# Kernel optimization log

Measured on AMD Instinct MI355X. Metric: run time of the kernel, lower is better.

Reference implementation:

```python
import jax, jax.numpy as jnp
import numpy as np

N = 100000      # nodes
E = 1600000     # edges
F = 64          # num_features
C = 10          # num_classes
L = 4           # num_layers
B = 128         # graphs in batch


def setup_inputs() -> dict:
    key = jax.random.key(0)
    ks = jax.random.split(key, 8)
    x = jax.random.normal(ks[0], (N, F), dtype=jnp.float32)
    edge_index = jax.random.randint(ks[1], (2, E), 0, N, dtype=jnp.int64)
    batch = jnp.sort(jax.random.randint(ks[2], (N,), 0, B, dtype=jnp.int64))
    scale = 1.0 / jnp.sqrt(jnp.float32(F))
    W1s = jax.random.normal(ks[3], (L, F, F), dtype=jnp.float32) * scale
    W2s = jax.random.normal(ks[4], (L, F, F), dtype=jnp.float32) * scale
    fc_w = jax.random.normal(ks[5], (C, F), dtype=jnp.float32) * scale
    fc_b = jax.random.normal(ks[6], (C,), dtype=jnp.float32) * 0.01
    return {"x": x, "edge_index": edge_index, "batch": batch,
            "W1s": W1s, "W2s": W2s, "fc_w": fc_w, "fc_b": fc_b}


def reference(x, edge_index, batch, W1s, W2s, fc_w, fc_b):
    src, dst = edge_index[0], edge_index[1]
    h = x
    for l in range(L):  # small fixed layer count
        # GINConv, eps=0: (1+eps)*x + sum of neighbor features (gather + scatter-add)
        agg = jax.ops.segment_sum(h[src], dst, num_segments=N)
        h = agg + h
        # MLP([F,F,F], bias=False, plain_last=False, act=sigmoid): two linears, each followed by sigmoid
        h = jax.nn.sigmoid(h @ W1s[l])
        h = jax.nn.sigmoid(h @ W2s[l])
    # global_add_pool over graphs in the batch
    xr = jax.ops.segment_sum(h, batch, num_segments=B)  # [B, F]
    logits = xr @ fc_w.T + fc_b                          # [B, C]
    return jax.nn.log_softmax(logits, axis=1), xr
```

## Files before the change

### kernel.cpp

```cpp
#include <hip/hip_runtime.h>
#include <hip/hip_bf16.h>

#define NN 100000
#define NE 1600000
#define FF 64
#define NC 10
#define NL 4
#define NB 128
#define LDST 72
#define CAP 48
#define NW 196
#define WCAPE 8704
#define PB_BIN 196
#define PB_XF 782
#define PB_W 32
#define PB_TOTAL (PB_BIN + PB_XF + PB_W + 1)
#define LAYER_BLOCKS ((NN + 15) / 16)

typedef __attribute__((ext_vector_type(8))) short short8;
typedef __attribute__((ext_vector_type(8))) unsigned short ushort8;
typedef __attribute__((ext_vector_type(4))) float f32x4;
typedef __attribute__((ext_vector_type(2))) float f32x2;
typedef __attribute__((ext_vector_type(4))) int int4v;

static __device__ __forceinline__ unsigned short f2bf(float x) {
  unsigned int u = __float_as_uint(x);
  unsigned int r = (u + 0x7fffu + ((u >> 16) & 1u)) >> 16;
  return (unsigned short)r;
}
static __device__ __forceinline__ float bf2f(unsigned short u) {
  return __uint_as_float(((unsigned int)u) << 16);
}
static __device__ __forceinline__ uint2 pack_f8(const float* a) {
  int w0 = __builtin_amdgcn_cvt_pk_fp8_f32(a[0], a[1], 0, false);
  w0 = __builtin_amdgcn_cvt_pk_fp8_f32(a[2], a[3], w0, true);
  int w1 = __builtin_amdgcn_cvt_pk_fp8_f32(a[4], a[5], 0, false);
  w1 = __builtin_amdgcn_cvt_pk_fp8_f32(a[6], a[7], w1, true);
  return make_uint2((unsigned)w0, (unsigned)w1);
}
static __device__ __forceinline__ void acc8w(f32x2* a, unsigned int x,
                                             unsigned int y) {
#if __has_builtin(__builtin_amdgcn_cvt_pk_f32_fp8)
  a[0] += __builtin_amdgcn_cvt_pk_f32_fp8((int)x, false);
  a[1] += __builtin_amdgcn_cvt_pk_f32_fp8((int)x, true);
  a[2] += __builtin_amdgcn_cvt_pk_f32_fp8((int)y, false);
  a[3] += __builtin_amdgcn_cvt_pk_f32_fp8((int)y, true);
#else
  a[0][0] += __builtin_amdgcn_cvt_f32_fp8((int)x, 0);
  a[0][1] += __builtin_amdgcn_cvt_f32_fp8((int)x, 1);
  a[1][0] += __builtin_amdgcn_cvt_f32_fp8((int)x, 2);
  a[1][1] += __builtin_amdgcn_cvt_f32_fp8((int)x, 3);
  a[2][0] += __builtin_amdgcn_cvt_f32_fp8((int)y, 0);
  a[2][1] += __builtin_amdgcn_cvt_f32_fp8((int)y, 1);
  a[3][0] += __builtin_amdgcn_cvt_f32_fp8((int)y, 2);
  a[3][1] += __builtin_amdgcn_cvt_f32_fp8((int)y, 3);
#endif
}
static __device__ __forceinline__ void acc16(f32x2* a, uint4 v) {
  acc8w(a, v.x, v.y);
  acc8w(a + 4, v.z, v.w);
}
static __device__ __forceinline__ void nacc(unsigned& pe0, unsigned& po0,
                                            unsigned& pe1, unsigned& po1,
                                            uint2 r) {
  pe0 += r.x & 0x0F0F0F0Fu; po0 += (r.x >> 4) & 0x0F0F0F0Fu;
  pe1 += r.y & 0x0F0F0F0Fu; po1 += (r.y >> 4) & 0x0F0F0F0Fu;
}

__global__ __launch_bounds__(1024) void prepbin_kernel(
    const float* __restrict__ x, const int* __restrict__ src,
    const int* __restrict__ dst, const float* __restrict__ W1s,
    const float* __restrict__ W2s, uint2* __restrict__ xf8,
    unsigned short* __restrict__ Wt, int* __restrict__ wcnt,
    unsigned int* __restrict__ ebuf, unsigned char* __restrict__ hq0,
    unsigned char* __restrict__ hq1) {
  __shared__ int lcnt[NW];
  __shared__ int lbase[NW];
  int b = blockIdx.x;
  int t = threadIdx.x;
  if (b < PB_BIN) {
    int base = b * 8192 + t * 8;
    int d[8], s[8], wj[8], p8[8];
    bool v[8];
    if (base + 8 <= NE) {
      *(int4*)(&d[0]) = *(const int4*)(dst + base);
      *(int4*)(&d[4]) = *(const int4*)(dst + base + 4);
      *(int4*)(&s[0]) = *(const int4*)(src + base);
      *(int4*)(&s[4]) = *(const int4*)(src + base + 4);
      #pragma unroll
      for (int j = 0; j < 8; ++j) v[j] = true;
    } else {
      #pragma unroll
      for (int j = 0; j < 8; ++j) {
        int e = base + j;
        v[j] = (e < NE);
        d[j] = v[j] ? dst[e] : 0;
        s[j] = v[j] ? src[e] : 0;
      }
    }
    #pragma unroll
    for (int j = 0; j < 8; ++j) wj[j] = d[j] >> 9;
    if (t < NW) lcnt[t] = 0;
    __syncthreads();
    #pragma unroll
    for (int j = 0; j < 8; ++j)
      if (v[j]) p8[j] = atomicAdd(&lcnt[wj[j]], 1);
    __syncthreads();
    if (t < NW) lbase[t] = atomicAdd(&wcnt[t], lcnt[t]);
    __syncthreads();
    #pragma unroll
    for (int j = 0; j < 8; ++j) {
      if (v[j]) {
        int pos = lbase[wj[j]] + p8[j];
        if (pos < WCAPE)
          ebuf[(size_t)wj[j] * WCAPE + pos] =
              ((unsigned)(d[j] & 511) << 17) | (unsigned)s[j];
      }
    }
  } else if (b < PB_BIN + PB_XF) {
    int g = (b - PB_BIN) * 1024 + t;
    if (g < NN * FF / 8) {
      size_t base = (size_t)g * 8;
      float4 a = *(const float4*)(x + base);
      float4 c = *(const float4*)(x + base + 4);
      float f[8] = {a.x, a.y, a.z, a.w, c.x, c.y, c.z, c.w};
      xf8[g] = pack_f8(f);
    }
  } else if (b < PB_BIN + PB_XF + PB_W) {
    int g = (b - PB_BIN - PB_XF) * 1024 + t;
    int mat = g >> 12, idx = g & 4095;
    int k = idx >> 6, n = idx & 63;
    int l = mat >> 1;
    const float* W = (mat & 1) ? (W2s + (size_t)l * FF * FF) : (W1s + (size_t)l * FF * FF);
    Wt[(size_t)mat * FF * FF + n * FF + k] = f2bf(W[k * FF + n]);
  } else {
    if (t < 8) {
      xf8[(size_t)NN * 8 + t] = make_uint2(0, 0);
    } else if (t < 12) {
      ((uint2*)hq0)[(size_t)NN * 4 + (t - 8)] = make_uint2(0, 0);
    } else if (t < 16) {
      ((uint2*)hq1)[(size_t)NN * 4 + (t - 12)] = make_uint2(0, 0);
    }
  }
}

__global__ __launch_bounds__(1024) void fillC_kernel(const unsigned int* __restrict__ ebuf,
                                                     const int* __restrict__ wcnt,
                                                     int* __restrict__ csr,
                                                     int* __restrict__ deg) {
  __shared__ int cur[512];
  int b = blockIdx.x;
  int t = threadIdx.x;
  int n0 = b << 9;
  if (t < 512) cur[t] = 0;
  __syncthreads();
  int cnt = min(wcnt[b], WCAPE);
  const unsigned int* ep = ebuf + (size_t)b * WCAPE;
  for (int i = t; i < cnt; i += 1024) {
    unsigned int e = ep[i];
    int dl = e >> 17;
    int s = (int)(e & 0x1ffffu);
    int slot = atomicAdd(&cur[dl], 1);
    if (slot < CAP) csr[(n0 + dl) * CAP + slot] = s;
  }
  __syncthreads();
  if (t < 512) {
    int node = n0 + t;
    if (node < NN) {
      int c = min(cur[t], CAP);
      deg[node] = c;
      int end = (c + 3) & ~3;
      for (; c < end; ++c) csr[node * CAP + c] = NN;
    }
  }
}

template <int IN4>
__global__ __launch_bounds__(64) void layer_kernel(
    const void* __restrict__ hin, const int* __restrict__ csr,
    const int* __restrict__ deg, const unsigned short* __restrict__ Wt,
    unsigned char* __restrict__ hout4, const int* __restrict__ batch,
    float* __restrict__ xr, int last) {
  __shared__ __align__(16) unsigned short uL[16 * LDST];
  __shared__ __align__(16) unsigned char fb[16 * 64];
  int lane = threadIdx.x;
  int row0 = blockIdx.x * 16;
  int j2 = lane & 3;
  int gnode = lane >> 2;

  {
    int r = gnode;
    int node = row0 + r;
    ushort8 u0, u1;
    if (IN4) {
      float af[16];
      #pragma unroll
      for (int k = 0; k < 16; ++k) af[k] = 0.f;
      if (node < NN) {
        const uint2* hb = (const uint2*)hin;
        uint2 sv = hb[(size_t)node * 4 + j2];
        unsigned se0 = sv.x & 0x0F0F0F0Fu, so0 = (sv.x >> 4) & 0x0F0F0F0Fu;
        unsigned se1 = sv.y & 0x0F0F0F0Fu, so1 = (sv.y >> 4) & 0x0F0F0F0Fu;
        #pragma unroll
        for (int k = 0; k < 4; ++k) {
          af[2 * k]         = (float)((se0 >> (8 * k)) & 0xFFu);
          af[2 * k + 1]     = (float)((so0 >> (8 * k)) & 0xFFu);
          af[8 + 2 * k]     = (float)((se1 >> (8 * k)) & 0xFFu);
          af[8 + 2 * k + 1] = (float)((so1 >> (8 * k)) & 0xFFu);
        }
        int i = node * CAP;
        int dg = deg[node];
        int endp = i + ((dg + 3) & ~3);
        while (i < endp) {
          unsigned pe0 = 0, po0 = 0, pe1 = 0, po1 = 0;
          int stop = min(endp, i + 16);
          for (; i + 8 <= stop; i += 8) {
            int4v x0 = *(const int4v*)(csr + i);
            int4v x1 = *(const int4v*)(csr + i + 4);
            uint2 r0 = hb[(size_t)x0[0] * 4 + j2];
            uint2 r1 = hb[(size_t)x0[1] * 4 + j2];
            uint2 r2 = hb[(size_t)x0[2] * 4 + j2];
            uint2 r3 = hb[(size_t)x0[3] * 4 + j2];
            uint2 r4 = hb[(size_t)x1[0] * 4 + j2];
            uint2 r5 = hb[(size_t)x1[1] * 4 + j2];
            uint2 r6 = hb[(size_t)x1[2] * 4 + j2];
            uint2 r7 = hb[(size_t)x1[3] * 4 + j2];
            nacc(pe0, po0, pe1, po1, r0); nacc(pe0, po0, pe1, po1, r1);
            nacc(pe0, po0, pe1, po1, r2); nacc(pe0, po0, pe1, po1, r3);
            nacc(pe0, po0, pe1, po1, r4); nacc(pe0, po0, pe1, po1, r5);
            nacc(pe0, po0, pe1, po1, r6); nacc(pe0, po0, pe1, po1, r7);
          }
          if (i < stop) {
            int4v x0 = *(const int4v*)(csr + i);
            uint2 r0 = hb[(size_t)x0[0] * 4 + j2];
            uint2 r1 = hb[(size_t)x0[1] * 4 + j2];
            uint2 r2 = hb[(size_t)x0[2] * 4 + j2];
            uint2 r3 = hb[(size_t)x0[3] * 4 + j2];
            nacc(pe0, po0, pe1, po1, r0); nacc(pe0, po0, pe1, po1, r1);
            nacc(pe0, po0, pe1, po1, r2); nacc(pe0, po0, pe1, po1, r3);
            i += 4;
          }
          #pragma unroll
          for (int k = 0; k < 4; ++k) {
            af[2 * k]         += (float)((pe0 >> (8 * k)) & 0xFFu);
            af[2 * k + 1]     += (float)((po0 >> (8 * k)) & 0xFFu);
            af[8 + 2 * k]     += (float)((pe1 >> (8 * k)) & 0xFFu);
            af[8 + 2 * k + 1] += (float)((po1 >> (8 * k)) & 0xFFu);
          }
        }
      }
      const float S = 1.f / 15.f;
      #pragma unroll
      for (int kk = 0; kk < 8; ++kk) u0[kk] = f2bf(af[kk] * S);
      #pragma unroll
      for (int kk = 0; kk < 8; ++kk) u1[kk] = f2bf(af[8 + kk] * S);
    } else {
      f32x2 a[8] = {{0.f,0.f},{0.f,0.f},{0.f,0.f},{0.f,0.f},
                    {0.f,0.f},{0.f,0.f},{0.f,0.f},{0.f,0.f}};
      const uint4* hp4 = (const uint4*)hin + j2;
      if (node < NN) {
        acc16(a, hp4[(size_t)node * 4]);
        int i = node * CAP;
        int dg = deg[node];
        int endp = i + ((dg + 3) & ~3);
        int4v nxt = *(const int4v*)(csr + i);
        while (i < endp) {
          int4v cur = nxt;
          nxt = *(const int4v*)(csr + i + 4);
          uint4 r0 = hp4[(size_t)cur[0] * 4];
          uint4 r1 = hp4[(size_t)cur[1] * 4];
          uint4 r2 = hp4[(size_t)cur[2] * 4];
          uint4 r3 = hp4[(size_t)cur[3] * 4];
          acc16(a, r0); acc16(a, r1); acc16(a, r2); acc16(a, r3);
          i += 4;
        }
      }
      #pragma unroll
      for (int kk = 0; kk < 8; ++kk) u0[kk] = f2bf(a[kk >> 1][kk & 1]);
      #pragma unroll
      for (int kk = 0; kk < 8; ++kk) u1[kk] = f2bf(a[4 + (kk >> 1)][kk & 1]);
    }
    *(ushort8*)(&uL[r * LDST + j2 * 16]) = u0;
    *(ushort8*)(&uL[r * LDST + j2 * 16 + 8]) = u1;
  }

  __builtin_amdgcn_sched_barrier(0);

  int m = lane & 15, q = lane >> 4;
  short8 b1[4][2], b2[4][2];
  #pragma unroll
  for (int c4 = 0; c4 < 4; ++c4) {
    #pragma unroll
    for (int s = 0; s < 2; ++s) {
      b1[c4][s] = *(const short8*)(Wt + (c4 * 16 + m) * FF + s * 32 + q * 8);
      b2[c4][s] = *(const short8*)(Wt + FF * FF + (c4 * 16 + m) * FF + s * 32 + q * 8);
    }
  }

  f32x4 acc[4] = {{0,0,0,0},{0,0,0,0},{0,0,0,0},{0,0,0,0}};
  #pragma unroll
  for (int s = 0; s < 2; ++s) {
    short8 a = *(const short8*)(&uL[m * LDST + s * 32 + q * 8]);
    #pragma unroll
    for (int c4 = 0; c4 < 4; ++c4)
      acc[c4] = __builtin_amdgcn_mfma_f32_16x16x32_bf16(a, b1[c4][s], acc[c4], 0, 0, 0);
  }
  #pragma unroll
  for (int c4 = 0; c4 < 4; ++c4) {
    #pragma unroll
    for (int i = 0; i < 4; ++i) {
      int r = q * 4 + i;
      float sgv = 1.f / (1.f + __expf(-acc[c4][i]));
      uL[r * LDST + c4 * 16 + m] = f2bf(sgv);
    }
  }

  f32x4 acc2[4] = {{0,0,0,0},{0,0,0,0},{0,0,0,0},{0,0,0,0}};
  #pragma unroll
  for (int s = 0; s < 2; ++s) {
    short8 a = *(const short8*)(&uL[m * LDST + s * 32 + q * 8]);
    #pragma unroll
    for (int c4 = 0; c4 < 4; ++c4)
      acc2[c4] = __builtin_amdgcn_mfma_f32_16x16x32_bf16(a, b2[c4][s], acc2[c4], 0, 0, 0);
  }
  if (last) {
    #pragma unroll
    for (int c4 = 0; c4 < 4; ++c4) {
      #pragma unroll
      for (int i = 0; i < 4; ++i) {
        int r = q * 4 + i;
        float sgv = 1.f / (1.f + __expf(-acc2[c4][i]));
        uL[r * LDST + c4 * 16 + m] = f2bf(sgv);
      }
    }
    int node0 = row0;
    if (node0 < NN) {
      float pacc = 0.f;
      int cur = batch[node0];
      #pragma unroll
      for (int r = 0; r < 16; ++r) {
        int node = node0 + r;
        if (node < NN) {
          int bb = batch[node];
          if (bb != cur) {
            unsafeAtomicAdd(&xr[(size_t)cur * FF + lane], pacc);
            pacc = 0.f; cur = bb;
          }
          pacc += bf2f(uL[r * LDST + lane]);
        }
      }
      unsafeAtomicAdd(&xr[(size_t)cur * FF + lane], pacc);
    }
  } else {
    #pragma unroll
    for (int c4 = 0; c4 < 4; ++c4) {
      #pragma unroll
      for (int i = 0; i < 4; ++i) {
        int r = q * 4 + i;
        float sgv = 1.f / (1.f + __expf(-acc2[c4][i]));
        fb[r * 64 + c4 * 16 + m] = (unsigned char)(int)(sgv * 15.f + 0.5f);
      }
    }
    {
      int r = gnode;
      int node = row0 + r;
      if (node < NN) {
        const unsigned* fp = (const unsigned*)(fb + r * 64 + j2 * 16);
        unsigned x0 = fp[0], x1 = fp[1], x2 = fp[2], x3 = fp[3];
        unsigned t0 = x0 | (x0 >> 4), t1 = x1 | (x1 >> 4);
        unsigned t2 = x2 | (x2 >> 4), t3 = x3 | (x3 >> 4);
        unsigned lo = (t0 & 0xFFu) | ((t0 >> 8) & 0xFF00u) |
                      (((t1 & 0xFFu) | ((t1 >> 8) & 0xFF00u)) << 16);
        unsigned hi = (t2 & 0xFFu) | ((t2 >> 8) & 0xFF00u) |
                      (((t3 & 0xFFu) | ((t3 >> 8) & 0xFF00u)) << 16);
        *(uint2*)(hout4 + (size_t)node * 32 + j2 * 8) = make_uint2(lo, hi);
      }
    }
  }
}

__global__ __launch_bounds__(64) void head_kernel(
    const float* __restrict__ xr, const float* __restrict__ fcw,
    const float* __restrict__ fcb, float* __restrict__ out) {
  int b = blockIdx.x, lane = threadIdx.x;
  float v = xr[(size_t)b * FF + lane];
  out[NB * NC + (size_t)b * FF + lane] = v;
  float logit[NC];
  #pragma unroll
  for (int c = 0; c < NC; ++c) {
    float s = v * fcw[c * FF + lane];
    #pragma unroll
    for (int o = 32; o > 0; o >>= 1) s += __shfl_xor(s, o, 64);
    logit[c] = s + fcb[c];
  }
  float mx = logit[0];
  #pragma unroll
  for (int c = 1; c < NC; ++c) mx = fmaxf(mx, logit[c]);
  float se = 0.f;
  #pragma unroll
  for (int c = 0; c < NC; ++c) se += expf(logit[c] - mx);
  float lse = logf(se);
  if (lane < NC) out[b * NC + lane] = logit[lane] - mx - lse;
}

extern "C" void kernel_launch(void* const* d_in, const int* in_sizes, int n_in,
                              void* d_out, int out_size, void* d_ws, size_t ws_size,
                              hipStream_t stream) {
  const float* x     = (const float*)d_in[0];
  const int*   ei    = (const int*)d_in[1];
  const int*   batch = (const int*)d_in[2];
  const float* W1s   = (const float*)d_in[3];
  const float* W2s   = (const float*)d_in[4];
  const float* fcw   = (const float*)d_in[5];
  const float* fcb   = (const float*)d_in[6];
  float* out = (float*)d_out;

  char* p = (char*)d_ws;
  uint2* xf8 = (uint2*)p;          p += (size_t)(NN + 1) * 64;
  unsigned char* hq0 = (unsigned char*)p; p += (size_t)(NN + 1) * 32;
  unsigned char* hq1 = (unsigned char*)p; p += (size_t)(NN + 1) * 32;
  int* csr    = (int*)p;   p += (size_t)NN * CAP * 4;
  unsigned int* ebuf = (unsigned int*)p; p += (size_t)NW * WCAPE * 4;
  int* deg    = (int*)p;   p += (size_t)NN * 4;
  int* wcnt   = (int*)p;   p += (size_t)((NW + 63) & ~63) * 4;
  float* xr   = (float*)p; p += (size_t)NB * FF * 4;
  unsigned short* Wtall = (unsigned short*)p; p += (size_t)2 * NL * FF * FF * 2;

  const int* src = ei;
  const int* dst = ei + NE;

  hipMemsetAsync(wcnt, 0,
                 (size_t)((NW + 63) & ~63) * 4 + (size_t)NB * FF * 4, stream);

  prepbin_kernel<<<PB_TOTAL, 1024, 0, stream>>>(
      x, src, dst, W1s, W2s, xf8, Wtall, wcnt, ebuf, hq0, hq1);

  fillC_kernel<<<NW, 1024, 0, stream>>>(ebuf, wcnt, csr, deg);

  layer_kernel<0><<<LAYER_BLOCKS, 64, 0, stream>>>(
      (const void*)xf8, csr, deg, Wtall + 0 * 2 * FF * FF, hq0, batch, xr, 0);
  layer_kernel<1><<<LAYER_BLOCKS, 64, 0, stream>>>(
      (const void*)hq0, csr, deg, Wtall + 1 * 2 * FF * FF, hq1, batch, xr, 0);
  layer_kernel<1><<<LAYER_BLOCKS, 64, 0, stream>>>(
      (const void*)hq1, csr, deg, Wtall + 2 * 2 * FF * FF, hq0, batch, xr, 0);
  layer_kernel<1><<<LAYER_BLOCKS, 64, 0, stream>>>(
      (const void*)hq0, csr, deg, Wtall + 3 * 2 * FF * FF, hq1, batch, xr, 1);

  head_kernel<<<NB, 64, 0, stream>>>(xr, fcw, fcb, out);
}
```

Measured before the change: 235.9 us.

## Build CSR directly with global atomics, drop bin-then-fill kernel

```diff
diff --git a/kernel.cpp b/kernel.cpp
--- a/kernel.cpp
+++ b/kernel.cpp
@@ -9,8 +9,6 @@
 #define NB 128
 #define LDST 72
 #define CAP 48
-#define NW 196
-#define WCAPE 8704
 #define PB_BIN 196
 #define PB_XF 782
 #define PB_W 32
@@ -67,20 +65,18 @@
   pe1 += r.y & 0x0F0F0F0Fu; po1 += (r.y >> 4) & 0x0F0F0F0Fu;
 }
 
-__global__ __launch_bounds__(1024) void prepbin_kernel(
+__global__ __launch_bounds__(1024) void prepfill_kernel(
     const float* __restrict__ x, const int* __restrict__ src,
     const int* __restrict__ dst, const float* __restrict__ W1s,
     const float* __restrict__ W2s, uint2* __restrict__ xf8,
-    unsigned short* __restrict__ Wt, int* __restrict__ wcnt,
-    unsigned int* __restrict__ ebuf, unsigned char* __restrict__ hq0,
+    unsigned short* __restrict__ Wt, int* __restrict__ deg,
+    int* __restrict__ csr, unsigned char* __restrict__ hq0,
     unsigned char* __restrict__ hq1) {
-  __shared__ int lcnt[NW];
-  __shared__ int lbase[NW];
   int b = blockIdx.x;
   int t = threadIdx.x;
   if (b < PB_BIN) {
     int base = b * 8192 + t * 8;
-    int d[8], s[8], wj[8], p8[8];
+    int d[8], s[8];
     bool v[8];
     if (base + 8 <= NE) {
       *(int4*)(&d[0]) = *(const int4*)(dst + base);
@@ -99,22 +95,10 @@
       }
     }
     #pragma unroll
-    for (int j = 0; j < 8; ++j) wj[j] = d[j] >> 9;
-    if (t < NW) lcnt[t] = 0;
-    __syncthreads();
-    #pragma unroll
-    for (int j = 0; j < 8; ++j)
-      if (v[j]) p8[j] = atomicAdd(&lcnt[wj[j]], 1);
-    __syncthreads();
-    if (t < NW) lbase[t] = atomicAdd(&wcnt[t], lcnt[t]);
-    __syncthreads();
-    #pragma unroll
     for (int j = 0; j < 8; ++j) {
       if (v[j]) {
-        int pos = lbase[wj[j]] + p8[j];
-        if (pos < WCAPE)
-          ebuf[(size_t)wj[j] * WCAPE + pos] =
-              ((unsigned)(d[j] & 511) << 17) | (unsigned)s[j];
+        int slot = atomicAdd(&deg[d[j]], 1);
+        if (slot < CAP) csr[(size_t)d[j] * CAP + slot] = s[j];
       }
     }
   } else if (b < PB_BIN + PB_XF) {
@@ -144,37 +128,6 @@
   }
 }
 
-__global__ __launch_bounds__(1024) void fillC_kernel(const unsigned int* __restrict__ ebuf,
-                                                     const int* __restrict__ wcnt,
-                                                     int* __restrict__ csr,
-                                                     int* __restrict__ deg) {
-  __shared__ int cur[512];
-  int b = blockIdx.x;
-  int t = threadIdx.x;
-  int n0 = b << 9;
-  if (t < 512) cur[t] = 0;
-  __syncthreads();
-  int cnt = min(wcnt[b], WCAPE);
-  const unsigned int* ep = ebuf + (size_t)b * WCAPE;
-  for (int i = t; i < cnt; i += 1024) {
-    unsigned int e = ep[i];
-    int dl = e >> 17;
-    int s = (int)(e & 0x1ffffu);
-    int slot = atomicAdd(&cur[dl], 1);
-    if (slot < CAP) csr[(n0 + dl) * CAP + slot] = s;
-  }
-  __syncthreads();
-  if (t < 512) {
-    int node = n0 + t;
-    if (node < NN) {
-      int c = min(cur[t], CAP);
-      deg[node] = c;
-      int end = (c + 3) & ~3;
-      for (; c < end; ++c) csr[node * CAP + c] = NN;
-    }
-  }
-}
-
 template <int IN4>
 __global__ __launch_bounds__(64) void layer_kernel(
     const void* __restrict__ hin, const int* __restrict__ csr,
@@ -208,15 +161,16 @@
           af[8 + 2 * k]     = (float)((se1 >> (8 * k)) & 0xFFu);
           af[8 + 2 * k + 1] = (float)((so1 >> (8 * k)) & 0xFFu);
         }
-        int i = node * CAP;
-        int dg = deg[node];
-        int endp = i + ((dg + 3) & ~3);
-        while (i < endp) {
+        int dg = min(deg[node], CAP);
+        const int* cp = csr + node * CAP;
+        int nfull = dg >> 2, rem = dg & 3;
+        int q = 0;
+        while (q < nfull) {
           unsigned pe0 = 0, po0 = 0, pe1 = 0, po1 = 0;
-          int stop = min(endp, i + 16);
-          for (; i + 8 <= stop; i += 8) {
-            int4v x0 = *(const int4v*)(csr + i);
-            int4v x1 = *(const int4v*)(csr + i + 4);
+          int qstop = min(nfull, q + 4);
+          for (; q + 2 <= qstop; q += 2) {
+            int4v x0 = *(const int4v*)(cp + q * 4);
+            int4v x1 = *(const int4v*)(cp + q * 4 + 4);
             uint2 r0 = hb[(size_t)x0[0] * 4 + j2];
             uint2 r1 = hb[(size_t)x0[1] * 4 + j2];
             uint2 r2 = hb[(size_t)x0[2] * 4 + j2];
@@ -230,15 +184,15 @@
             nacc(pe0, po0, pe1, po1, r4); nacc(pe0, po0, pe1, po1, r5);
             nacc(pe0, po0, pe1, po1, r6); nacc(pe0, po0, pe1, po1, r7);
           }
-          if (i < stop) {
-            int4v x0 = *(const int4v*)(csr + i);
+          if (q < qstop) {
+            int4v x0 = *(const int4v*)(cp + q * 4);
             uint2 r0 = hb[(size_t)x0[0] * 4 + j2];
             uint2 r1 = hb[(size_t)x0[1] * 4 + j2];
             uint2 r2 = hb[(size_t)x0[2] * 4 + j2];
             uint2 r3 = hb[(size_t)x0[3] * 4 + j2];
             nacc(pe0, po0, pe1, po1, r0); nacc(pe0, po0, pe1, po1, r1);
             nacc(pe0, po0, pe1, po1, r2); nacc(pe0, po0, pe1, po1, r3);
-            i += 4;
+            ++q;
           }
           #pragma unroll
           for (int k = 0; k < 4; ++k) {
@@ -248,6 +202,25 @@
             af[8 + 2 * k + 1] += (float)((po1 >> (8 * k)) & 0xFFu);
           }
         }
+        if (rem) {
+          unsigned pe0 = 0, po0 = 0, pe1 = 0, po1 = 0;
+          int4v x0 = *(const int4v*)(cp + nfull * 4);
+          int i0 = x0[0];
+          int i1 = (rem > 1) ? x0[1] : NN;
+          int i2 = (rem > 2) ? x0[2] : NN;
+          uint2 r0 = hb[(size_t)i0 * 4 + j2];
+          uint2 r1 = hb[(size_t)i1 * 4 + j2];
+          uint2 r2 = hb[(size_t)i2 * 4 + j2];
+          nacc(pe0, po0, pe1, po1, r0); nacc(pe0, po0, pe1, po1, r1);
+          nacc(pe0, po0, pe1, po1, r2);
+          #pragma unroll
+          for (int k = 0; k < 4; ++k) {
+            af[2 * k]         += (float)((pe0 >> (8 * k)) & 0xFFu);
+            af[2 * k + 1]     += (float)((po0 >> (8 * k)) & 0xFFu);
+            af[8 + 2 * k]     += (float)((pe1 >> (8 * k)) & 0xFFu);
+            af[8 + 2 * k + 1] += (float)((po1 >> (8 * k)) & 0xFFu);
+          }
+        }
       }
       const float S = 1.f / 15.f;
       #pragma unroll
@@ -260,19 +233,26 @@
       const uint4* hp4 = (const uint4*)hin + j2;
       if (node < NN) {
         acc16(a, hp4[(size_t)node * 4]);
-        int i = node * CAP;
-        int dg = deg[node];
-        int endp = i + ((dg + 3) & ~3);
-        int4v nxt = *(const int4v*)(csr + i);
-        while (i < endp) {
-          int4v cur = nxt;
-          nxt = *(const int4v*)(csr + i + 4);
-          uint4 r0 = hp4[(size_t)cur[0] * 4];
-          uint4 r1 = hp4[(size_t)cur[1] * 4];
-          uint4 r2 = hp4[(size_t)cur[2] * 4];
-          uint4 r3 = hp4[(size_t)cur[3] * 4];
+        int dg = min(deg[node], CAP);
+        const int* cp = csr + node * CAP;
+        int nfull = dg >> 2, rem = dg & 3;
+        for (int q = 0; q < nfull; ++q) {
+          int4v x0 = *(const int4v*)(cp + q * 4);
+          uint4 r0 = hp4[(size_t)x0[0] * 4];
+          uint4 r1 = hp4[(size_t)x0[1] * 4];
+          uint4 r2 = hp4[(size_t)x0[2] * 4];
+          uint4 r3 = hp4[(size_t)x0[3] * 4];
           acc16(a, r0); acc16(a, r1); acc16(a, r2); acc16(a, r3);
-          i += 4;
+        }
+        if (rem) {
+          int4v x0 = *(const int4v*)(cp + nfull * 4);
+          int i0 = x0[0];
+          int i1 = (rem > 1) ? x0[1] : NN;
+          int i2 = (rem > 2) ? x0[2] : NN;
+          uint4 r0 = hp4[(size_t)i0 * 4];
+          uint4 r1 = hp4[(size_t)i1 * 4];
+          uint4 r2 = hp4[(size_t)i2 * 4];
+          acc16(a, r0); acc16(a, r1); acc16(a, r2);
         }
       }
       #pragma unroll
@@ -420,22 +400,17 @@
   unsigned char* hq0 = (unsigned char*)p; p += (size_t)(NN + 1) * 32;
   unsigned char* hq1 = (unsigned char*)p; p += (size_t)(NN + 1) * 32;
   int* csr    = (int*)p;   p += (size_t)NN * CAP * 4;
-  unsigned int* ebuf = (unsigned int*)p; p += (size_t)NW * WCAPE * 4;
   int* deg    = (int*)p;   p += (size_t)NN * 4;
-  int* wcnt   = (int*)p;   p += (size_t)((NW + 63) & ~63) * 4;
   float* xr   = (float*)p; p += (size_t)NB * FF * 4;
   unsigned short* Wtall = (unsigned short*)p; p += (size_t)2 * NL * FF * FF * 2;
 
   const int* src = ei;
   const int* dst = ei + NE;
 
-  hipMemsetAsync(wcnt, 0,
-                 (size_t)((NW + 63) & ~63) * 4 + (size_t)NB * FF * 4, stream);
-
-  prepbin_kernel<<<PB_TOTAL, 1024, 0, stream>>>(
-      x, src, dst, W1s, W2s, xf8, Wtall, wcnt, ebuf, hq0, hq1);
-
-  fillC_kernel<<<NW, 1024, 0, stream>>>(ebuf, wcnt, csr, deg);
+  hipMemsetAsync(deg, 0, (size_t)NN * 4 + (size_t)NB * FF * 4, stream);
+
+  prepfill_kernel<<<PB_TOTAL, 1024, 0, stream>>>(
+      x, src, dst, W1s, W2s, xf8, Wtall, deg, csr, hq0, hq1);
 
   layer_kernel<0><<<LAYER_BLOCKS, 64, 0, stream>>>(
       (const void*)xf8, csr, deg, Wtall + 0 * 2 * FF * FF, hq0, batch, xr, 0);
```

New measurement: 287.4 us. 21.8% more time.
